# Kernel optimization log

Measured on AMD Instinct MI355X. Metric: run time of the kernel, lower is better.

## Reference

```python
import jax, jax.numpy as jnp
import numpy as np

N, E, IN, HID, HEADS, ED, OUT = 50000, 600000, 128, 64, 4, 16, 2
NEG_SLOPE = 0.2  # PyG GATv2Conv default negative_slope


def glorot(key, shape):
    fan_in, fan_out = shape[0], shape[-1]
    s = jnp.sqrt(6.0 / (fan_in + fan_out))
    return jax.random.uniform(key, shape, jnp.float32, -s, s)


def setup_inputs() -> dict:
    key = jax.random.key(0)
    ks = jax.random.split(key, 16)
    return {
        "x": jax.random.normal(ks[0], (N, IN), jnp.float32),
        "edge_index": jax.random.randint(ks[1], (2, E), 0, N, jnp.int32),
        "edge_attr": jax.random.normal(ks[2], (E, ED), jnp.float32),
        # conv1: GATv2Conv(IN -> HID, heads=HEADS, concat=True, edge_dim=ED)
        "W1l": glorot(ks[3], (IN, HEADS * HID)), "b1l": jnp.zeros((HEADS * HID,), jnp.float32),
        "W1r": glorot(ks[4], (IN, HEADS * HID)), "b1r": jnp.zeros((HEADS * HID,), jnp.float32),
        "W1e": glorot(ks[5], (ED, HEADS * HID)), "b1e": jnp.zeros((HEADS * HID,), jnp.float32),
        "att1": glorot(ks[6], (HEADS, HID)),
        "bias1": jnp.zeros((HEADS * HID,), jnp.float32),
        # conv2: GATv2Conv(HEADS*HID -> HID, heads=1, concat=False, edge_dim=ED)
        "W2l": glorot(ks[7], (HEADS * HID, HID)), "b2l": jnp.zeros((HID,), jnp.float32),
        "W2r": glorot(ks[8], (HEADS * HID, HID)), "b2r": jnp.zeros((HID,), jnp.float32),
        "W2e": glorot(ks[9], (ED, HID)), "b2e": jnp.zeros((HID,), jnp.float32),
        "att2": glorot(ks[10], (1, HID)),
        "bias2": jnp.zeros((HID,), jnp.float32),
        # edge MLP: Linear(2*HID+ED -> HID) -> ReLU -> Linear(HID -> OUT)
        "Wm1": glorot(ks[11], (2 * HID + ED, HID)), "bm1": jnp.zeros((HID,), jnp.float32),
        "Wm2": glorot(ks[12], (HID, OUT)), "bm2": jnp.zeros((OUT,), jnp.float32),
    }


def gatv2_layer(x, src, dst, edge_attr, Wl, bl, Wr, br, We, be, att, bias, heads, ch, concat):
    n = x.shape[0]
    xl = (x @ Wl + bl).reshape(n, heads, ch)          # lin_l(source)
    xr = (x @ Wr + br).reshape(n, heads, ch)          # lin_r(target)
    xe = (edge_attr @ We + be).reshape(-1, heads, ch)  # lin_edge(edge_attr)
    m = jax.nn.leaky_relu(xl[src] + xr[dst] + xe, NEG_SLOPE)   # [E, H, C]
    logits = jnp.einsum('ehc,hc->eh', m, att)                  # [E, H]
    # segment softmax over incoming edges of each target node
    amax = jax.lax.stop_gradient(jax.ops.segment_max(logits, dst, num_segments=n))
    ex = jnp.exp(logits - amax[dst])
    denom = jax.ops.segment_sum(ex, dst, num_segments=n)
    alpha = ex / denom[dst]                                    # [E, H]
    out = jax.ops.segment_sum(xl[src] * alpha[..., None], dst, num_segments=n)  # [N, H, C]
    out = out.reshape(n, heads * ch) if concat else out.mean(axis=1)
    return out + bias


def reference(x, edge_index, edge_attr, W1l, b1l, W1r, b1r, W1e, b1e, att1, bias1,
              W2l, b2l, W2r, b2r, W2e, b2e, att2, bias2, Wm1, bm1, Wm2, bm2):
    src, dst = edge_index[0], edge_index[1]
    h = jax.nn.relu(gatv2_layer(x, src, dst, edge_attr, W1l, b1l, W1r, b1r, W1e, b1e, att1, bias1, HEADS, HID, True))
    h = jax.nn.relu(gatv2_layer(h, src, dst, edge_attr, W2l, b2l, W2r, b2r, W2e, b2e, att2, bias2, 1, HID, False))
    ef = jnp.concatenate([h[src], h[dst], edge_attr], axis=1)  # [E, 2*HID+ED]
    return jax.nn.relu(ef @ Wm1 + bm1) @ Wm2 + bm2             # [E, OUT]
```

## Files before the change

### kernel.cpp

```cpp
#include <hip/hip_runtime.h>
#include <math.h>

#define NN 50000
#define EE 600000
#define IND 128
#define HIDD 64
#define NH 4
#define EDD 16
#define OUTD 2
#define C1 256

typedef _Float16 h2 __attribute__((ext_vector_type(2)));

__device__ __forceinline__ unsigned short f2bf(float f){
    unsigned b = __float_as_uint(f);
    b += 0x7FFF + ((b >> 16) & 1);
    return (unsigned short)(b >> 16);
}
__device__ __forceinline__ float bf2f(unsigned short h){
    return __uint_as_float(((unsigned)h) << 16);
}
__device__ __forceinline__ h2 f2h2(float a, float b){
    h2 r; r[0] = (_Float16)a; r[1] = (_Float16)b; return r;
}

#if defined(__has_builtin)
#if __has_builtin(__builtin_amdgcn_fdot2)
#define HAS_FDOT2 1
#endif
#if __has_builtin(__builtin_amdgcn_exp2f)
#define HAS_EXP2 1
#endif
#endif
__device__ __forceinline__ float fdot2(h2 a, h2 b, float c){
#ifdef HAS_FDOT2
    return __builtin_amdgcn_fdot2(a, b, c, false);
#else
    return fmaf((float)a[1], (float)b[1], fmaf((float)a[0], (float)b[0], c));
#endif
}
__device__ __forceinline__ float fexp2(float x){
#ifdef HAS_EXP2
    return __builtin_amdgcn_exp2f(x);
#else
    return __expf(x * 0.69314718056f);
#endif
}

__global__ __launch_bounds__(256) void k_hist(const int* __restrict__ dst, int* __restrict__ cnt)
{
    int stride = gridDim.x * blockDim.x;
    for (int e = blockIdx.x * blockDim.x + threadIdx.x; e < EE; e += stride)
        atomicAdd(&cnt[dst[e]], 1);
}

__global__ __launch_bounds__(1024) void k_scan(const int* __restrict__ cnt, int* __restrict__ rs)
{
    __shared__ int wsum[16];
    __shared__ int wpref[16];
    int t = threadIdx.x, lane = t & 63, w = t >> 6;
    int running = 0;
    for (int base = 0; base < NN; base += 1024) {
        int idx = base + t;
        int v = (idx < NN) ? cnt[idx] : 0;
        int sc = v;
#pragma unroll
        for (int off = 1; off < 64; off <<= 1) {
            int u = __shfl_up(sc, off, 64);
            if (lane >= off) sc += u;
        }
        if (lane == 63) wsum[w] = sc;
        __syncthreads();
        if (w == 0 && lane < 16) {
            int x = wsum[lane];
#pragma unroll
            for (int off = 1; off < 16; off <<= 1) {
                int u = __shfl_up(x, off, 64);
                if (lane >= off) x += u;
            }
            wpref[lane] = x;
        }
        __syncthreads();
        int woff = (w == 0) ? 0 : wpref[w - 1];
        if (idx < NN) rs[idx] = running + woff + sc - v;
        running += wpref[15];
        __syncthreads();
    }
    if (t == 0) rs[NN] = running;
}

__global__ __launch_bounds__(256) void k_scatter_lin1(
    const int* __restrict__ src, const int* __restrict__ dst,
    const float* __restrict__ ea,
    const int* __restrict__ rs, int* __restrict__ cur,
    int* __restrict__ esrc, _Float16* __restrict__ ea_s, _Float16* __restrict__ ea_h,
    const float* __restrict__ x, const float* __restrict__ Wl, const float* __restrict__ bl,
    const float* __restrict__ Wr, const float* __restrict__ br,
    unsigned short* __restrict__ xl, float* __restrict__ xr)
{
    __shared__ h2 As[32 * 64];
    if (blockIdx.x < 1024) {
        int stride = 1024 * 256;
        for (int e = blockIdx.x * 256 + threadIdx.x; e < EE; e += stride) {
            int d = dst[e];
            int p = rs[d] + atomicAdd(&cur[d], 1);
            esrc[p] = src[e];
            const float4* s4 = (const float4*)(ea + (size_t)e * EDD);
            float4 a0 = s4[0], a1 = s4[1], a2 = s4[2], a3 = s4[3];
            union { h2 h[8]; uint4 u[2]; } pk;
            pk.h[0] = f2h2(a0.x, a0.y); pk.h[1] = f2h2(a0.z, a0.w);
            pk.h[2] = f2h2(a1.x, a1.y); pk.h[3] = f2h2(a1.z, a1.w);
            pk.h[4] = f2h2(a2.x, a2.y); pk.h[5] = f2h2(a2.z, a2.w);
            pk.h[6] = f2h2(a3.x, a3.y); pk.h[7] = f2h2(a3.z, a3.w);
            uint4* dq = (uint4*)(ea_s + (size_t)p * EDD);
            dq[0] = pk.u[0]; dq[1] = pk.u[1];
            uint4* hq = (uint4*)(ea_h + (size_t)e * EDD);
            hq[0] = pk.u[0]; hq[1] = pk.u[1];
        }
        return;
    }
    int t = threadIdx.x;
    int row0 = (blockIdx.x - 1024) * 32;
#pragma unroll
    for (int j = 0; j < 4; ++j) {
        int idx = t + j * 256;
        int r = idx >> 5, c4 = (idx & 31) * 4;
        float4 v = (row0 + r < NN) ? *((const float4*)(x + (size_t)(row0 + r) * IND + c4))
                                   : make_float4(0.f, 0.f, 0.f, 0.f);
        union { h2 h[2]; uint2 u; } pk;
        pk.h[0] = f2h2(v.x, v.y); pk.h[1] = f2h2(v.z, v.w);
        *((uint2*)&As[r * 64 + (c4 >> 1)]) = pk.u;
    }
    __syncthreads();
    float accl[32], accr[32];
    float bL = bl[t], bR = br[t];
#pragma unroll
    for (int i = 0; i < 32; ++i) { accl[i] = bL; accr[i] = bR; }
    for (int k = 0; k < IND; k += 4) {
        h2 wl01 = f2h2(Wl[(k+0) * C1 + t], Wl[(k+1) * C1 + t]);
        h2 wl23 = f2h2(Wl[(k+2) * C1 + t], Wl[(k+3) * C1 + t]);
        h2 wr01 = f2h2(Wr[(k+0) * C1 + t], Wr[(k+1) * C1 + t]);
        h2 wr23 = f2h2(Wr[(k+2) * C1 + t], Wr[(k+3) * C1 + t]);
#pragma unroll
        for (int i = 0; i < 32; ++i) {
            union { uint2 u; h2 h[2]; } av;
            av.u = *((const uint2*)&As[i * 64 + (k >> 1)]);
            accl[i] = fdot2(av.h[0], wl01, accl[i]);
            accl[i] = fdot2(av.h[1], wl23, accl[i]);
            accr[i] = fdot2(av.h[0], wr01, accr[i]);
            accr[i] = fdot2(av.h[1], wr23, accr[i]);
        }
    }
#pragma unroll
    for (int i = 0; i < 32; ++i) {
        int r = row0 + i;
        if (r < NN) {
            xl[(size_t)r * C1 + t] = f2bf(accl[i]);
            xr[(size_t)r * C1 + t] = accr[i];
        }
    }
}

#define GAT1_E(XU, U0, U1) {                                                   \
    float4 xl4 = make_float4(bf2f((XU).x), bf2f((XU).y), bf2f((XU).z), bf2f((XU).w)); \
    union { uint4 u[2]; h2 h[8]; } eu_; eu_.u[0] = (U0); eu_.u[1] = (U1);      \
    float zx = xrb4.x, zy = xrb4.y, zz = xrb4.z, zw = xrb4.w;                  \
    _Pragma("unroll")                                                          \
    for (int kk = 0; kk < 8; ++kk) {                                           \
        h2 ev2 = eu_.h[kk];                                                    \
        zx = fdot2(ev2, Wh[0][kk], zx);                                        \
        zy = fdot2(ev2, Wh[1][kk], zy);                                        \
        zz = fdot2(ev2, Wh[2][kk], zz);                                        \
        zw = fdot2(ev2, Wh[3][kk], zw);                                        \
    }                                                                          \
    zx += xl4.x; zy += xl4.y; zz += xl4.z; zw += xl4.w;                        \
    float vx = fmaxf(zx, 0.2f * zx);                                           \
    float vy = fmaxf(zy, 0.2f * zy);                                           \
    float vz = fmaxf(zz, 0.2f * zz);                                           \
    float vw = fmaxf(zw, 0.2f * zw);                                           \
    float p = vx * sa4.x + vy * sa4.y + vz * sa4.z + vw * sa4.w;               \
    p += __shfl_xor(p, 1, 64);                                                 \
    p += __shfl_xor(p, 2, 64);                                                 \
    p += __shfl_xor(p, 4, 64);                                                 \
    p += __shfl_xor(p, 8, 64);                                                 \
    float el = fexp2(p);                                                       \
    den += el;                                                                 \
    acc.x = fmaf(el, xl4.x, acc.x);                                            \
    acc.y = fmaf(el, xl4.y, acc.y);                                            \
    acc.z = fmaf(el, xl4.z, acc.z);                                            \
    acc.w = fmaf(el, xl4.w, acc.w);                                            \
}

__global__ __launch_bounds__(256) void k_gat1(
    const int* __restrict__ rs, const int* __restrict__ esrc,
    const _Float16* __restrict__ ea_s, const float* __restrict__ We, const float* __restrict__ be,
    const float* __restrict__ att, const unsigned short* __restrict__ xl,
    const float* __restrict__ xr, float* __restrict__ h1)
{
    int t = threadIdx.x, lane = t & 63, w = t >> 6;
    int c4 = lane * 4;
    h2 Wh[4][8];
#pragma unroll
    for (int k = 0; k < 16; ++k) {
        float4 wv = *((const float4*)(We + k * C1 + c4));
        Wh[0][k>>1][k&1] = (_Float16)wv.x;
        Wh[1][k>>1][k&1] = (_Float16)wv.y;
        Wh[2][k>>1][k&1] = (_Float16)wv.z;
        Wh[3][k>>1][k&1] = (_Float16)wv.w;
    }
    float4 sb4 = *((const float4*)(be + c4));
    float4 sa4 = *((const float4*)(att + c4));
    sa4.x *= 1.44269504f; sa4.y *= 1.44269504f;
    sa4.z *= 1.44269504f; sa4.w *= 1.44269504f;
    for (int n = blockIdx.x * 4 + w; n < NN; n += gridDim.x * 4) {
        int beg = __builtin_amdgcn_readfirstlane(rs[n]);
        int end = __builtin_amdgcn_readfirstlane(rs[n + 1]);
        float4 xr4 = *((const float4*)(xr + (size_t)n * C1 + c4));
        float4 xrb4 = make_float4(sb4.x + xr4.x, sb4.y + xr4.y,
                                  sb4.z + xr4.z, sb4.w + xr4.w);
        float den = 0.f;
        float4 acc = make_float4(0.f, 0.f, 0.f, 0.f);
        int i = beg;
        for (; i + 4 <= end; i += 4) {
            int s0 = esrc[i], s1 = esrc[i + 1], s2 = esrc[i + 2], s3 = esrc[i + 3];
            ushort4 xu0 = *((const ushort4*)(xl + (size_t)s0 * C1 + c4));
            ushort4 xu1 = *((const ushort4*)(xl + (size_t)s1 * C1 + c4));
            ushort4 xu2 = *((const ushort4*)(xl + (size_t)s2 * C1 + c4));
            ushort4 xu3 = *((const ushort4*)(xl + (size_t)s3 * C1 + c4));
            const uint4* ep = (const uint4*)(ea_s + (size_t)i * EDD);
            uint4 u0 = ep[0], u1 = ep[1], u2 = ep[2], u3 = ep[3];
            uint4 u4 = ep[4], u5 = ep[5], u6 = ep[6], u7 = ep[7];
            GAT1_E(xu0, u0, u1);
            GAT1_E(xu1, u2, u3);
            GAT1_E(xu2, u4, u5);
            GAT1_E(xu3, u6, u7);
        }
        for (; i < end; ++i) {
            int s0 = esrc[i];
            ushort4 xu0 = *((const ushort4*)(xl + (size_t)s0 * C1 + c4));
            const uint4* ep = (const uint4*)(ea_s + (size_t)i * EDD);
            uint4 u00 = ep[0], u01 = ep[1];
            GAT1_E(xu0, u00, u01);
        }
        float r = den > 0.f ? 1.f / den : 0.f;
        float4 o = make_float4(acc.x * r, acc.y * r, acc.z * r, acc.w * r);
        *((float4*)(h1 + (size_t)n * C1 + c4)) = o;
    }
}

__global__ __launch_bounds__(256) void k_lin2(
    const float* __restrict__ h1acc, const float* __restrict__ bias1,
    const float* __restrict__ Wl, const float* __restrict__ bl,
    const float* __restrict__ Wr, const float* __restrict__ br,
    unsigned short* __restrict__ xl2, float* __restrict__ xr2)
{
    __shared__ h2 As[32 * 130];
    int t = threadIdx.x;
    int row0 = blockIdx.x * 32;
    float b1v = bias1[t];
#pragma unroll
    for (int j = 0; j < 32; ++j) {
        float v = (row0 + j < NN) ? h1acc[(size_t)(row0 + j) * C1 + t] : 0.f;
        v = v + b1v;
        v = v > 0.f ? v : 0.f;
        As[j * 130 + (t >> 1)][t & 1] = (_Float16)v;
    }
    __syncthreads();
    int col = t & 63, g = t >> 6;
    float accl[8], accr[8];
    float bL = bl[col], bR = br[col];
#pragma unroll
    for (int i = 0; i < 8; ++i) { accl[i] = bL; accr[i] = bR; }
    for (int k = 0; k < C1; k += 4) {
        h2 wl01 = f2h2(Wl[(k+0) * HIDD + col], Wl[(k+1) * HIDD + col]);
        h2 wl23 = f2h2(Wl[(k+2) * HIDD + col], Wl[(k+3) * HIDD + col]);
        h2 wr01 = f2h2(Wr[(k+0) * HIDD + col], Wr[(k+1) * HIDD + col]);
        h2 wr23 = f2h2(Wr[(k+2) * HIDD + col], Wr[(k+3) * HIDD + col]);
#pragma unroll
        for (int i = 0; i < 8; ++i) {
            union { uint2 u; h2 h[2]; } av;
            av.u = *((const uint2*)&As[(g * 8 + i) * 130 + (k >> 1)]);
            accl[i] = fdot2(av.h[0], wl01, accl[i]);
            accl[i] = fdot2(av.h[1], wl23, accl[i]);
            accr[i] = fdot2(av.h[0], wr01, accr[i]);
            accr[i] = fdot2(av.h[1], wr23, accr[i]);
        }
    }
#pragma unroll
    for (int i = 0; i < 8; ++i) {
        int r = row0 + g * 8 + i;
        if (r < NN) {
            xl2[(size_t)r * HIDD + col] = f2bf(accl[i]);
            xr2[(size_t)r * HIDD + col] = accr[i];
        }
    }
}

__global__ __launch_bounds__(256) void k_gat2(
    const int* __restrict__ rs, const int* __restrict__ esrc,
    const _Float16* __restrict__ ea_s, const float* __restrict__ We, const float* __restrict__ be,
    const float* __restrict__ att, const unsigned short* __restrict__ xl,
    const float* __restrict__ xr, const float* __restrict__ bias2, float* __restrict__ h2v)
{
    int t = threadIdx.x, lane = t & 63, w = t >> 6;
    int sub = lane & 15, grp = lane >> 4;
    int c4 = sub * 4;
    h2 Wh[4][8];
#pragma unroll
    for (int k = 0; k < 16; ++k) {
        float4 wv = *((const float4*)(We + k * HIDD + c4));
        Wh[0][k>>1][k&1] = (_Float16)wv.x;
        Wh[1][k>>1][k&1] = (_Float16)wv.y;
        Wh[2][k>>1][k&1] = (_Float16)wv.z;
        Wh[3][k>>1][k&1] = (_Float16)wv.w;
    }
    float4 be4 = *((const float4*)(be + c4));
    float4 sa4 = *((const float4*)(att + c4));
    sa4.x *= 1.44269504f; sa4.y *= 1.44269504f;
    sa4.z *= 1.44269504f; sa4.w *= 1.44269504f;
    float4 b24 = *((const float4*)(bias2 + c4));
    for (int n = blockIdx.x * 4 + w; n < NN; n += gridDim.x * 4) {
        int beg = __builtin_amdgcn_readfirstlane(rs[n]);
        int end = __builtin_amdgcn_readfirstlane(rs[n + 1]);
        float4 xr4 = *((const float4*)(xr + (size_t)n * HIDD + c4));
        float4 xrb4 = make_float4(be4.x + xr4.x, be4.y + xr4.y,
                                  be4.z + xr4.z, be4.w + xr4.w);
        float den = 0.f;
        float4 acc = make_float4(0.f, 0.f, 0.f, 0.f);
        for (int i = beg; i < end; i += 4) {
            int e = i + grp;
            int ec = e < end ? e : end - 1;
            int s = esrc[ec];
            ushort4 xu = *((const ushort4*)(xl + (size_t)s * HIDD + c4));
            const uint4* ep = (const uint4*)(ea_s + (size_t)ec * EDD);
            union { uint4 u[2]; h2 h[8]; } eu_;
            eu_.u[0] = ep[0]; eu_.u[1] = ep[1];
            float4 xl4 = make_float4(bf2f(xu.x), bf2f(xu.y), bf2f(xu.z), bf2f(xu.w));
            float zx = xrb4.x, zy = xrb4.y, zz = xrb4.z, zw = xrb4.w;
#pragma unroll
            for (int kk = 0; kk < 8; ++kk) {
                h2 ev2 = eu_.h[kk];
                zx = fdot2(ev2, Wh[0][kk], zx);
                zy = fdot2(ev2, Wh[1][kk], zy);
                zz = fdot2(ev2, Wh[2][kk], zz);
                zw = fdot2(ev2, Wh[3][kk], zw);
            }
            zx += xl4.x; zy += xl4.y; zz += xl4.z; zw += xl4.w;
            float vx = fmaxf(zx, 0.2f * zx);
            float vy = fmaxf(zy, 0.2f * zy);
            float vz = fmaxf(zz, 0.2f * zz);
            float vw = fmaxf(zw, 0.2f * zw);
            float p = vx * sa4.x + vy * sa4.y + vz * sa4.z + vw * sa4.w;
            p += __shfl_xor(p, 1, 64);
            p += __shfl_xor(p, 2, 64);
            p += __shfl_xor(p, 4, 64);
            p += __shfl_xor(p, 8, 64);
            float el = (e < end) ? fexp2(p) : 0.f;
            den += el;
            acc.x = fmaf(el, xl4.x, acc.x);
            acc.y = fmaf(el, xl4.y, acc.y);
            acc.z = fmaf(el, xl4.z, acc.z);
            acc.w = fmaf(el, xl4.w, acc.w);
        }
        den += __shfl_xor(den, 16, 64);
        den += __shfl_xor(den, 32, 64);
        acc.x += __shfl_xor(acc.x, 16, 64); acc.x += __shfl_xor(acc.x, 32, 64);
        acc.y += __shfl_xor(acc.y, 16, 64); acc.y += __shfl_xor(acc.y, 32, 64);
        acc.z += __shfl_xor(acc.z, 16, 64); acc.z += __shfl_xor(acc.z, 32, 64);
        acc.w += __shfl_xor(acc.w, 16, 64); acc.w += __shfl_xor(acc.w, 32, 64);
        float r = den > 0.f ? 1.f / den : 0.f;
        if (grp == 0) {
            float4 o;
            o.x = fmaxf(fmaf(acc.x, r, b24.x), 0.f);
            o.y = fmaxf(fmaf(acc.y, r, b24.y), 0.f);
            o.z = fmaxf(fmaf(acc.z, r, b24.z), 0.f);
            o.w = fmaxf(fmaf(acc.w, r, b24.w), 0.f);
            *((float4*)(h2v + (size_t)n * HIDD + c4)) = o;
        }
    }
}

__global__ __launch_bounds__(256) void k_pq(
    const float* __restrict__ h2, const float* __restrict__ Wm1,
    unsigned short* __restrict__ P, unsigned short* __restrict__ Q)
{
    __shared__ float As[16 * 68];
    int t = threadIdx.x;
    int row0 = blockIdx.x * 16;
    {
        int r = t >> 4, cc = (t & 15) * 4;
        float4 v = *((const float4*)(h2 + (size_t)(row0 + r) * HIDD + cc));
        *((float4*)&As[r * 68 + cc]) = v;
    }
    __syncthreads();
    int col = t & 63, g = t >> 6;
    float accP[4] = {0.f, 0.f, 0.f, 0.f}, accQ[4] = {0.f, 0.f, 0.f, 0.f};
    for (int k = 0; k < 64; k += 4) {
        float wp0 = Wm1[(k+0) * HIDD + col], wp1 = Wm1[(k+1) * HIDD + col];
        float wp2 = Wm1[(k+2) * HIDD + col], wp3 = Wm1[(k+3) * HIDD + col];
        float wq0 = Wm1[(64+k+0) * HIDD + col], wq1 = Wm1[(64+k+1) * HIDD + col];
        float wq2 = Wm1[(64+k+2) * HIDD + col], wq3 = Wm1[(64+k+3) * HIDD + col];
#pragma unroll
        for (int i = 0; i < 4; ++i) {
            float4 a = *((const float4*)&As[(g * 4 + i) * 68 + k]);
            accP[i] = fmaf(a.x, wp0, accP[i]); accP[i] = fmaf(a.y, wp1, accP[i]);
            accP[i] = fmaf(a.z, wp2, accP[i]); accP[i] = fmaf(a.w, wp3, accP[i]);
            accQ[i] = fmaf(a.x, wq0, accQ[i]); accQ[i] = fmaf(a.y, wq1, accQ[i]);
            accQ[i] = fmaf(a.z, wq2, accQ[i]); accQ[i] = fmaf(a.w, wq3, accQ[i]);
        }
    }
#pragma unroll
    for (int i = 0; i < 4; ++i) {
        int r = row0 + g * 4 + i;
        P[(size_t)r * HIDD + col] = f2bf(accP[i]);
        Q[(size_t)r * HIDD + col] = f2bf(accQ[i]);
    }
}

__global__ __launch_bounds__(256) void k_edge(
    const int* __restrict__ src, const int* __restrict__ dst,
    const unsigned short* __restrict__ P, const unsigned short* __restrict__ Q,
    const _Float16* __restrict__ ea_h,
    const float* __restrict__ Wm1, const float* __restrict__ bm1,
    const float* __restrict__ Wm2, const float* __restrict__ bm2,
    float* __restrict__ out)
{
    int t = threadIdx.x, lane = t & 63, w = t >> 6;
    int sub = lane & 15, grp = lane >> 4;
    int c4 = sub * 4;
    h2 Wh[4][8];
#pragma unroll
    for (int k = 0; k < 16; ++k) {
        float4 wv = *((const float4*)(Wm1 + (size_t)(128 + k) * HIDD + c4));
        Wh[0][k>>1][k&1] = (_Float16)wv.x;
        Wh[1][k>>1][k&1] = (_Float16)wv.y;
        Wh[2][k>>1][k&1] = (_Float16)wv.z;
        Wh[3][k>>1][k&1] = (_Float16)wv.w;
    }
    float4 b1 = *((const float4*)(bm1 + c4));
    float w200 = Wm2[(c4+0)*2], w201 = Wm2[(c4+0)*2+1];
    float w210 = Wm2[(c4+1)*2], w211 = Wm2[(c4+1)*2+1];
    float w220 = Wm2[(c4+2)*2], w221 = Wm2[(c4+2)*2+1];
    float w230 = Wm2[(c4+3)*2], w231 = Wm2[(c4+3)*2+1];
    float b20 = bm2[0], b21 = bm2[1];
    for (int base = blockIdx.x * 16 + w * 4; base < EE; base += gridDim.x * 16) {
        int e = base + grp;
        int s = src[e], d = dst[e];
        ushort4 pu = *((const ushort4*)(P + (size_t)s * HIDD + c4));
        ushort4 qu = *((const ushort4*)(Q + (size_t)d * HIDD + c4));
        union { uint4 u[2]; h2 h[8]; } eu_;
        const uint4* ep = (const uint4*)(ea_h + (size_t)e * EDD);
        eu_.u[0] = ep[0]; eu_.u[1] = ep[1];
        float4 hsum = b1;
#pragma unroll
        for (int kk = 0; kk < 8; ++kk) {
            h2 ev2 = eu_.h[kk];
            hsum.x = fdot2(ev2, Wh[0][kk], hsum.x);
            hsum.y = fdot2(ev2, Wh[1][kk], hsum.y);
            hsum.z = fdot2(ev2, Wh[2][kk], hsum.z);
            hsum.w = fdot2(ev2, Wh[3][kk], hsum.w);
        }
        float hx = fmaxf(hsum.x + bf2f(pu.x) + bf2f(qu.x), 0.f);
        float hy = fmaxf(hsum.y + bf2f(pu.y) + bf2f(qu.y), 0.f);
        float hz = fmaxf(hsum.z + bf2f(pu.z) + bf2f(qu.z), 0.f);
        float hw = fmaxf(hsum.w + bf2f(pu.w) + bf2f(qu.w), 0.f);
        float p0 = hx * w200 + hy * w210 + hz * w220 + hw * w230;
        float p1 = hx * w201 + hy * w211 + hz * w221 + hw * w231;
        p0 += __shfl_xor(p0, 1, 64);
        p0 += __shfl_xor(p0, 2, 64);
        p0 += __shfl_xor(p0, 4, 64);
        p0 += __shfl_xor(p0, 8, 64);
        p1 += __shfl_xor(p1, 1, 64);
        p1 += __shfl_xor(p1, 2, 64);
        p1 += __shfl_xor(p1, 4, 64);
        p1 += __shfl_xor(p1, 8, 64);
        if (sub == 0) ((float2*)out)[e] = make_float2(p0 + b20, p1 + b21);
    }
}

extern "C" void kernel_launch(void* const* d_in, const int* in_sizes, int n_in,
                              void* d_out, int out_size, void* d_ws, size_t ws_size,
                              hipStream_t stream)
{
    const float* x    = (const float*)d_in[0];
    const int*   ei   = (const int*)d_in[1];
    const float* ea   = (const float*)d_in[2];
    const float* W1l  = (const float*)d_in[3];
    const float* b1l  = (const float*)d_in[4];
    const float* W1r  = (const float*)d_in[5];
    const float* b1r  = (const float*)d_in[6];
    const float* W1e  = (const float*)d_in[7];
    const float* b1e  = (const float*)d_in[8];
    const float* att1 = (const float*)d_in[9];
    const float* bias1= (const float*)d_in[10];
    const float* W2l  = (const float*)d_in[11];
    const float* b2l  = (const float*)d_in[12];
    const float* W2r  = (const float*)d_in[13];
    const float* b2r  = (const float*)d_in[14];
    const float* W2e  = (const float*)d_in[15];
    const float* b2e  = (const float*)d_in[16];
    const float* att2 = (const float*)d_in[17];
    const float* bias2= (const float*)d_in[18];
    const float* Wm1  = (const float*)d_in[19];
    const float* bm1  = (const float*)d_in[20];
    const float* Wm2  = (const float*)d_in[21];
    const float* bm2  = (const float*)d_in[22];
    float* out = (float*)d_out;
    const int* srcp = ei;
    const int* dstp = ei + EE;

    float* ws = (float*)d_ws;
    const size_t NC1  = (size_t)NN * C1;
    const size_t NH64 = (size_t)NN * HIDD;
    const size_t EAH  = (size_t)EE * EDD / 2;
    size_t o_xl1u = 0;
    size_t o_xr1  = o_xl1u + NC1 / 2;
    size_t o_xl2u = 0;
    size_t o_xr2  = o_xl2u + NH64 / 2;
    size_t o_h2   = o_xr2 + NH64;
    size_t o_Pu   = o_h2 + NH64;
    size_t o_Qu   = o_Pu + NH64 / 2;
    size_t o_h1   = o_xr1 + NC1;
    size_t o_ea_s = o_h1 + NC1;
    size_t o_ea_h = o_ea_s + EAH;
    size_t o_cnt  = o_ea_h + EAH;
    size_t o_rs   = o_cnt + 2 * (size_t)NN;
    size_t o_esrc = o_rs + (size_t)NN + 8;

    unsigned short* xl1u = (unsigned short*)(ws + o_xl1u);
    unsigned short* xl2u = (unsigned short*)(ws + o_xl2u);
    unsigned short* Pu   = (unsigned short*)(ws + o_Pu);
    unsigned short* Qu   = (unsigned short*)(ws + o_Qu);
    _Float16* ea_s = (_Float16*)(ws + o_ea_s);
    _Float16* ea_h = (_Float16*)(ws + o_ea_h);
    int* cnt  = (int*)(ws + o_cnt);
    int* cur  = cnt + NN;
    int* rs   = (int*)(ws + o_rs);
    int* esrc = (int*)(ws + o_esrc);

    hipMemsetAsync(cnt, 0, 2 * (size_t)NN * sizeof(int), stream);

    dim3 blk(256);
    k_hist<<<1024, blk, 0, stream>>>(dstp, cnt);
    k_scan<<<1, 1024, 0, stream>>>(cnt, rs);
    k_scatter_lin1<<<2587, blk, 0, stream>>>(srcp, dstp, ea, rs, cur, esrc,
                                             ea_s, ea_h,
                                             x, W1l, b1l, W1r, b1r,
                                             xl1u, ws + o_xr1);
    k_gat1<<<2048, blk, 0, stream>>>(rs, esrc, ea_s, W1e, b1e, att1,
                                     xl1u, ws + o_xr1, ws + o_h1);
    k_lin2<<<1563, blk, 0, stream>>>(ws + o_h1, bias1, W2l, b2l, W2r, b2r,
                                     xl2u, ws + o_xr2);
    k_gat2<<<2048, blk, 0, stream>>>(rs, esrc, ea_s, W2e, b2e, att2,
                                     xl2u, ws + o_xr2, bias2, ws + o_h2);
    k_pq<<<3125, blk, 0, stream>>>(ws + o_h2, Wm1, Pu, Qu);
    k_edge<<<2048, blk, 0, stream>>>(srcp, dstp, Pu, Qu, ea_h,
                                     Wm1, bm1, Wm2, bm2, out);
}
```

Baseline: 592.7 us.

## Replace sorted edge-attr copy with (src, edge id) pairs and indirect gather

Stops writing a CSR-sorted copy of the half-precision edge attributes during the scatter. The scatter now stores a (source, original edge id) pair per sorted slot, and the fp32-to-fp16 conversion of edge attributes moves into the histogram kernel. Both GAT kernels then gather the 32-byte edge attribute rows indirectly by edge id. This removes one scattered write stream and halves the conversion work in the scatter kernel, but turns contiguous edge-attribute reads in the GAT kernels into random gathers and doubles the index array size.

```diff
diff --git a/kernel.cpp b/kernel.cpp
--- a/kernel.cpp
+++ b/kernel.cpp
@@ -47,11 +47,23 @@
 #endif
 }
 
-__global__ __launch_bounds__(256) void k_hist(const int* __restrict__ dst, int* __restrict__ cnt)
+__global__ __launch_bounds__(256) void k_hist_cvt(
+    const int* __restrict__ dst, int* __restrict__ cnt,
+    const float* __restrict__ ea, _Float16* __restrict__ ea_h)
 {
     int stride = gridDim.x * blockDim.x;
-    for (int e = blockIdx.x * blockDim.x + threadIdx.x; e < EE; e += stride)
+    for (int e = blockIdx.x * blockDim.x + threadIdx.x; e < EE; e += stride) {
         atomicAdd(&cnt[dst[e]], 1);
+        const float4* s4 = (const float4*)(ea + (size_t)e * EDD);
+        float4 a0 = s4[0], a1 = s4[1], a2 = s4[2], a3 = s4[3];
+        union { h2 h[8]; uint4 u[2]; } pk;
+        pk.h[0] = f2h2(a0.x, a0.y); pk.h[1] = f2h2(a0.z, a0.w);
+        pk.h[2] = f2h2(a1.x, a1.y); pk.h[3] = f2h2(a1.z, a1.w);
+        pk.h[4] = f2h2(a2.x, a2.y); pk.h[5] = f2h2(a2.z, a2.w);
+        pk.h[6] = f2h2(a3.x, a3.y); pk.h[7] = f2h2(a3.z, a3.w);
+        uint4* hq = (uint4*)(ea_h + (size_t)e * EDD);
+        hq[0] = pk.u[0]; hq[1] = pk.u[1];
+    }
 }
 
 __global__ __launch_bounds__(1024) void k_scan(const int* __restrict__ cnt, int* __restrict__ rs)
@@ -91,9 +103,8 @@
 
 __global__ __launch_bounds__(256) void k_scatter_lin1(
     const int* __restrict__ src, const int* __restrict__ dst,
-    const float* __restrict__ ea,
     const int* __restrict__ rs, int* __restrict__ cur,
-    int* __restrict__ esrc, _Float16* __restrict__ ea_s, _Float16* __restrict__ ea_h,
+    int2* __restrict__ ese,
     const float* __restrict__ x, const float* __restrict__ Wl, const float* __restrict__ bl,
     const float* __restrict__ Wr, const float* __restrict__ br,
     unsigned short* __restrict__ xl, float* __restrict__ xr)
@@ -104,18 +115,7 @@
         for (int e = blockIdx.x * 256 + threadIdx.x; e < EE; e += stride) {
             int d = dst[e];
             int p = rs[d] + atomicAdd(&cur[d], 1);
-            esrc[p] = src[e];
-            const float4* s4 = (const float4*)(ea + (size_t)e * EDD);
-            float4 a0 = s4[0], a1 = s4[1], a2 = s4[2], a3 = s4[3];
-            union { h2 h[8]; uint4 u[2]; } pk;
-            pk.h[0] = f2h2(a0.x, a0.y); pk.h[1] = f2h2(a0.z, a0.w);
-            pk.h[2] = f2h2(a1.x, a1.y); pk.h[3] = f2h2(a1.z, a1.w);
-            pk.h[4] = f2h2(a2.x, a2.y); pk.h[5] = f2h2(a2.z, a2.w);
-            pk.h[6] = f2h2(a3.x, a3.y); pk.h[7] = f2h2(a3.z, a3.w);
-            uint4* dq = (uint4*)(ea_s + (size_t)p * EDD);
-            dq[0] = pk.u[0]; dq[1] = pk.u[1];
-            uint4* hq = (uint4*)(ea_h + (size_t)e * EDD);
-            hq[0] = pk.u[0]; hq[1] = pk.u[1];
+            ese[p] = make_int2(src[e], e);
         }
         return;
     }
@@ -192,8 +192,8 @@
 }
 
 __global__ __launch_bounds__(256) void k_gat1(
-    const int* __restrict__ rs, const int* __restrict__ esrc,
-    const _Float16* __restrict__ ea_s, const float* __restrict__ We, const float* __restrict__ be,
+    const int* __restrict__ rs, const int2* __restrict__ ese,
+    const _Float16* __restrict__ ea_h, const float* __restrict__ We, const float* __restrict__ be,
     const float* __restrict__ att, const unsigned short* __restrict__ xl,
     const float* __restrict__ xr, float* __restrict__ h1)
 {
@@ -222,24 +222,29 @@
         float4 acc = make_float4(0.f, 0.f, 0.f, 0.f);
         int i = beg;
         for (; i + 4 <= end; i += 4) {
-            int s0 = esrc[i], s1 = esrc[i + 1], s2 = esrc[i + 2], s3 = esrc[i + 3];
-            ushort4 xu0 = *((const ushort4*)(xl + (size_t)s0 * C1 + c4));
-            ushort4 xu1 = *((const ushort4*)(xl + (size_t)s1 * C1 + c4));
-            ushort4 xu2 = *((const ushort4*)(xl + (size_t)s2 * C1 + c4));
-            ushort4 xu3 = *((const ushort4*)(xl + (size_t)s3 * C1 + c4));
-            const uint4* ep = (const uint4*)(ea_s + (size_t)i * EDD);
-            uint4 u0 = ep[0], u1 = ep[1], u2 = ep[2], u3 = ep[3];
-            uint4 u4 = ep[4], u5 = ep[5], u6 = ep[6], u7 = ep[7];
+            int2 v0 = ese[i], v1 = ese[i + 1], v2 = ese[i + 2], v3 = ese[i + 3];
+            ushort4 xu0 = *((const ushort4*)(xl + (size_t)v0.x * C1 + c4));
+            ushort4 xu1 = *((const ushort4*)(xl + (size_t)v1.x * C1 + c4));
+            ushort4 xu2 = *((const ushort4*)(xl + (size_t)v2.x * C1 + c4));
+            ushort4 xu3 = *((const ushort4*)(xl + (size_t)v3.x * C1 + c4));
+            const uint4* e0 = (const uint4*)(ea_h + (size_t)v0.y * EDD);
+            const uint4* e1 = (const uint4*)(ea_h + (size_t)v1.y * EDD);
+            const uint4* e2 = (const uint4*)(ea_h + (size_t)v2.y * EDD);
+            const uint4* e3 = (const uint4*)(ea_h + (size_t)v3.y * EDD);
+            uint4 u0 = e0[0], u1 = e0[1];
+            uint4 u2 = e1[0], u3 = e1[1];
+            uint4 u4 = e2[0], u5 = e2[1];
+            uint4 u6 = e3[0], u7 = e3[1];
             GAT1_E(xu0, u0, u1);
             GAT1_E(xu1, u2, u3);
             GAT1_E(xu2, u4, u5);
             GAT1_E(xu3, u6, u7);
         }
         for (; i < end; ++i) {
-            int s0 = esrc[i];
-            ushort4 xu0 = *((const ushort4*)(xl + (size_t)s0 * C1 + c4));
-            const uint4* ep = (const uint4*)(ea_s + (size_t)i * EDD);
-            uint4 u00 = ep[0], u01 = ep[1];
+            int2 v0 = ese[i];
+            ushort4 xu0 = *((const ushort4*)(xl + (size_t)v0.x * C1 + c4));
+            const uint4* e0 = (const uint4*)(ea_h + (size_t)v0.y * EDD);
+            uint4 u00 = e0[0], u01 = e0[1];
             GAT1_E(xu0, u00, u01);
         }
         float r = den > 0.f ? 1.f / den : 0.f;
@@ -297,8 +302,8 @@
 }
 
 __global__ __launch_bounds__(256) void k_gat2(
-    const int* __restrict__ rs, const int* __restrict__ esrc,
-    const _Float16* __restrict__ ea_s, const float* __restrict__ We, const float* __restrict__ be,
+    const int* __restrict__ rs, const int2* __restrict__ ese,
+    const _Float16* __restrict__ ea_h, const float* __restrict__ We, const float* __restrict__ be,
     const float* __restrict__ att, const unsigned short* __restrict__ xl,
     const float* __restrict__ xr, const float* __restrict__ bias2, float* __restrict__ h2v)
 {
@@ -330,9 +335,9 @@
         for (int i = beg; i < end; i += 4) {
             int e = i + grp;
             int ec = e < end ? e : end - 1;
-            int s = esrc[ec];
-            ushort4 xu = *((const ushort4*)(xl + (size_t)s * HIDD + c4));
-            const uint4* ep = (const uint4*)(ea_s + (size_t)ec * EDD);
+            int2 v = ese[ec];
+            ushort4 xu = *((const ushort4*)(xl + (size_t)v.x * HIDD + c4));
+            const uint4* ep = (const uint4*)(ea_h + (size_t)v.y * EDD);
             union { uint4 u[2]; h2 h[8]; } eu_;
             eu_.u[0] = ep[0]; eu_.u[1] = ep[1];
             float4 xl4 = make_float4(bf2f(xu.x), bf2f(xu.y), bf2f(xu.z), bf2f(xu.w));
@@ -521,8 +526,8 @@
     size_t o_Pu   = o_h2 + NH64;
     size_t o_Qu   = o_Pu + NH64 / 2;
     size_t o_h1   = o_xr1 + NC1;
-    size_t o_ea_s = o_h1 + NC1;
-    size_t o_ea_h = o_ea_s + EAH;
+    size_t o_ese  = o_h1 + NC1;
+    size_t o_ea_h = o_ese + EAH;
     size_t o_cnt  = o_ea_h + EAH;
     size_t o_rs   = o_cnt + 2 * (size_t)NN;
     size_t o_esrc = o_rs + (size_t)NN + 8;
@@ -531,27 +536,26 @@
     unsigned short* xl2u = (unsigned short*)(ws + o_xl2u);
     unsigned short* Pu   = (unsigned short*)(ws + o_Pu);
     unsigned short* Qu   = (unsigned short*)(ws + o_Qu);
-    _Float16* ea_s = (_Float16*)(ws + o_ea_s);
+    int2* ese = (int2*)(ws + o_ese);
     _Float16* ea_h = (_Float16*)(ws + o_ea_h);
     int* cnt  = (int*)(ws + o_cnt);
     int* cur  = cnt + NN;
     int* rs   = (int*)(ws + o_rs);
-    int* esrc = (int*)(ws + o_esrc);
+    (void)o_esrc;
 
     hipMemsetAsync(cnt, 0, 2 * (size_t)NN * sizeof(int), stream);
 
     dim3 blk(256);
-    k_hist<<<1024, blk, 0, stream>>>(dstp, cnt);
+    k_hist_cvt<<<1024, blk, 0, stream>>>(dstp, cnt, ea, ea_h);
     k_scan<<<1, 1024, 0, stream>>>(cnt, rs);
-    k_scatter_lin1<<<2587, blk, 0, stream>>>(srcp, dstp, ea, rs, cur, esrc,
-                                             ea_s, ea_h,
+    k_scatter_lin1<<<2587, blk, 0, stream>>>(srcp, dstp, rs, cur, ese,
                                              x, W1l, b1l, W1r, b1r,
                                              xl1u, ws + o_xr1);
-    k_gat1<<<2048, blk, 0, stream>>>(rs, esrc, ea_s, W1e, b1e, att1,
+    k_gat1<<<2048, blk, 0, stream>>>(rs, ese, ea_h, W1e, b1e, att1,
                                      xl1u, ws + o_xr1, ws + o_h1);
     k_lin2<<<1563, blk, 0, stream>>>(ws + o_h1, bias1, W2l, b2l, W2r, b2r,
                                      xl2u, ws + o_xr2);
-    k_gat2<<<2048, blk, 0, stream>>>(rs, esrc, ea_s, W2e, b2e, att2,
+    k_gat2<<<2048, blk, 0, stream>>>(rs, ese, ea_h, W2e, b2e, att2,
                                      xl2u, ws + o_xr2, bias2, ws + o_h2);
     k_pq<<<3125, blk, 0, stream>>>(ws + o_h2, Wm1, Pu, Qu);
     k_edge<<<2048, blk, 0, stream>>>(srcp, dstp, Pu, Qu, ea_h,
```

Measured after the change: 606.7 us. +2.4%, slower.

## Fuse P/Q projection into GAT layer-2 aggregation kernel

Applied to the files above, without the earlier changes.

Removes the separate k_pq kernel. k_gat2 now loads the two 64x64 halves of Wm1 into shared memory, transposed, and computes the P and Q bf16 rows from each node's h2 output directly inside the wave. This skips writing and re-reading the fp32 h2 buffer and saves one kernel launch. The cost is about 35KB of LDS per block, which may lower occupancy for the latency-bound gather kernel. The per-wave shared hrow write and read relies on wave-synchronous execution with no barrier.

```diff
diff --git a/kernel.cpp b/kernel.cpp
--- a/kernel.cpp
+++ b/kernel.cpp
@@ -300,9 +300,20 @@
     const int* __restrict__ rs, const int* __restrict__ esrc,
     const _Float16* __restrict__ ea_s, const float* __restrict__ We, const float* __restrict__ be,
     const float* __restrict__ att, const unsigned short* __restrict__ xl,
-    const float* __restrict__ xr, const float* __restrict__ bias2, float* __restrict__ h2v)
-{
+    const float* __restrict__ xr, const float* __restrict__ bias2,
+    const float* __restrict__ Wm1,
+    unsigned short* __restrict__ P, unsigned short* __restrict__ Q)
+{
+    __shared__ float WmP[64 * 68];
+    __shared__ float WmQ[64 * 68];
+    __shared__ float hrow[4][64];
     int t = threadIdx.x, lane = t & 63, w = t >> 6;
+    for (int idx = t; idx < 64 * 64; idx += 256) {
+        int k = idx >> 6, col = idx & 63;
+        WmP[col * 68 + k] = Wm1[k * HIDD + col];
+        WmQ[col * 68 + k] = Wm1[(64 + k) * HIDD + col];
+    }
+    __syncthreads();
     int sub = lane & 15, grp = lane >> 4;
     int c4 = sub * 4;
     h2 Wh[4][8];
@@ -369,51 +380,28 @@
         acc.z += __shfl_xor(acc.z, 16, 64); acc.z += __shfl_xor(acc.z, 32, 64);
         acc.w += __shfl_xor(acc.w, 16, 64); acc.w += __shfl_xor(acc.w, 32, 64);
         float r = den > 0.f ? 1.f / den : 0.f;
-        if (grp == 0) {
-            float4 o;
-            o.x = fmaxf(fmaf(acc.x, r, b24.x), 0.f);
-            o.y = fmaxf(fmaf(acc.y, r, b24.y), 0.f);
-            o.z = fmaxf(fmaf(acc.z, r, b24.z), 0.f);
-            o.w = fmaxf(fmaf(acc.w, r, b24.w), 0.f);
-            *((float4*)(h2v + (size_t)n * HIDD + c4)) = o;
-        }
-    }
-}
-
-__global__ __launch_bounds__(256) void k_pq(
-    const float* __restrict__ h2, const float* __restrict__ Wm1,
-    unsigned short* __restrict__ P, unsigned short* __restrict__ Q)
-{
-    __shared__ float As[16 * 68];
-    int t = threadIdx.x;
-    int row0 = blockIdx.x * 16;
-    {
-        int r = t >> 4, cc = (t & 15) * 4;
-        float4 v = *((const float4*)(h2 + (size_t)(row0 + r) * HIDD + cc));
-        *((float4*)&As[r * 68 + cc]) = v;
-    }
-    __syncthreads();
-    int col = t & 63, g = t >> 6;
-    float accP[4] = {0.f, 0.f, 0.f, 0.f}, accQ[4] = {0.f, 0.f, 0.f, 0.f};
-    for (int k = 0; k < 64; k += 4) {
-        float wp0 = Wm1[(k+0) * HIDD + col], wp1 = Wm1[(k+1) * HIDD + col];
-        float wp2 = Wm1[(k+2) * HIDD + col], wp3 = Wm1[(k+3) * HIDD + col];
-        float wq0 = Wm1[(64+k+0) * HIDD + col], wq1 = Wm1[(64+k+1) * HIDD + col];
-        float wq2 = Wm1[(64+k+2) * HIDD + col], wq3 = Wm1[(64+k+3) * HIDD + col];
-#pragma unroll
-        for (int i = 0; i < 4; ++i) {
-            float4 a = *((const float4*)&As[(g * 4 + i) * 68 + k]);
-            accP[i] = fmaf(a.x, wp0, accP[i]); accP[i] = fmaf(a.y, wp1, accP[i]);
-            accP[i] = fmaf(a.z, wp2, accP[i]); accP[i] = fmaf(a.w, wp3, accP[i]);
-            accQ[i] = fmaf(a.x, wq0, accQ[i]); accQ[i] = fmaf(a.y, wq1, accQ[i]);
-            accQ[i] = fmaf(a.z, wq2, accQ[i]); accQ[i] = fmaf(a.w, wq3, accQ[i]);
-        }
-    }
-#pragma unroll
-    for (int i = 0; i < 4; ++i) {
-        int r = row0 + g * 4 + i;
-        P[(size_t)r * HIDD + col] = f2bf(accP[i]);
-        Q[(size_t)r * HIDD + col] = f2bf(accQ[i]);
+        float4 o;
+        o.x = fmaxf(fmaf(acc.x, r, b24.x), 0.f);
+        o.y = fmaxf(fmaf(acc.y, r, b24.y), 0.f);
+        o.z = fmaxf(fmaf(acc.z, r, b24.z), 0.f);
+        o.w = fmaxf(fmaf(acc.w, r, b24.w), 0.f);
+        if (grp == 0) *((float4*)&hrow[w][c4]) = o;
+        float accP = 0.f, accQ = 0.f;
+        const float* hp = &hrow[w][0];
+        const float* wp = &WmP[lane * 68];
+        const float* wq = &WmQ[lane * 68];
+#pragma unroll
+        for (int k = 0; k < 64; k += 4) {
+            float4 hv = *((const float4*)&hp[k]);
+            float4 pv = *((const float4*)&wp[k]);
+            float4 qv = *((const float4*)&wq[k]);
+            accP = fmaf(hv.x, pv.x, accP); accP = fmaf(hv.y, pv.y, accP);
+            accP = fmaf(hv.z, pv.z, accP); accP = fmaf(hv.w, pv.w, accP);
+            accQ = fmaf(hv.x, qv.x, accQ); accQ = fmaf(hv.y, qv.y, accQ);
+            accQ = fmaf(hv.z, qv.z, accQ); accQ = fmaf(hv.w, qv.w, accQ);
+        }
+        P[(size_t)n * HIDD + lane] = f2bf(accP);
+        Q[(size_t)n * HIDD + lane] = f2bf(accQ);
     }
 }
 
@@ -552,8 +540,7 @@
     k_lin2<<<1563, blk, 0, stream>>>(ws + o_h1, bias1, W2l, b2l, W2r, b2r,
                                      xl2u, ws + o_xr2);
     k_gat2<<<2048, blk, 0, stream>>>(rs, esrc, ea_s, W2e, b2e, att2,
-                                     xl2u, ws + o_xr2, bias2, ws + o_h2);
-    k_pq<<<3125, blk, 0, stream>>>(ws + o_h2, Wm1, Pu, Qu);
+                                     xl2u, ws + o_xr2, bias2, Wm1, Pu, Qu);
     k_edge<<<2048, blk, 0, stream>>>(srcp, dstp, Pu, Qu, ea_h,
                                      Wm1, bm1, Wm2, bm2, out);
 }
```

After: 632.7 us. +6.8%, slower.
